# Kernel tuning notes

Hardware: AMD Instinct MI355X
Metric: run time of the kernel (lower is better)

The kernel has to match this reference:

```python
import jax, jax.numpy as jnp
import numpy as np


def setup_inputs() -> dict:
    key = jax.random.key(0)
    ks = jax.random.split(key, 8)
    B, QL, CL = 4, 128, 512
    XD, ED, D, YD = 64, 128, 128, 32
    sc = lambda fan_in: 1.0 / np.sqrt(fan_in)
    return {
        "q": jax.random.normal(ks[0], (B, QL, XD), jnp.float32),
        "f_embed": jax.random.normal(ks[1], (B, CL, ED), jnp.float32),
        "att_logits": jax.random.normal(ks[2], (B, QL, CL), jnp.float32),
        "W0": jax.random.normal(ks[3], (XD + ED, D), jnp.float32) * sc(XD + ED),
        "b0": jnp.zeros((D,), jnp.float32),
        "W1": jax.random.normal(ks[4], (D, D), jnp.float32) * sc(D),
        "b1": jnp.zeros((D,), jnp.float32),
        "Wo": jax.random.normal(ks[5], (D, YD), jnp.float32) * sc(D),
        "bo": jnp.zeros((YD,), jnp.float32),
    }


def reference(q, f_embed, att_logits, W0, b0, W1, b1, Wo, bo):
    # MultiInputDense on (qq, ff_embed): concat along last dim -> Dense(relu) x2 -> Dense(y_dim).
    # Split the first matmul so we never materialize the tiled concat:
    # concat([qq, ff]) @ W0 == qq @ W0[:xd] + ff @ W0[xd:]
    xd = q.shape[-1]
    q_part = jnp.einsum('bqx,xd->bqd', q, W0[:xd])          # [B, q_len, dim]
    f_part = jnp.einsum('bce,ed->bcd', f_embed, W0[xd:])    # [B, context_len, dim]
    h = jax.nn.relu(q_part[:, :, None, :] + f_part[:, None, :, :] + b0)  # [B,q,c,dim]
    h = jax.nn.relu(jnp.einsum('bqcd,de->bqce', h, W1) + b1)             # [B,q,c,dim]
    yy_hat = jnp.einsum('bqcd,dy->bqcy', h, Wo) + bo                     # [B,q,c,y_dim]
    att_map = jax.nn.softmax(att_logits, axis=-1)                        # [B,q,c]
    y_hat = jnp.einsum('bqc,bqcy->bqy', att_map, yy_hat)                 # [B,q,y_dim]
    return y_hat
```

## Files before the change

### kernel.cpp

```cpp
#include <hip/hip_runtime.h>

#define B_  4
#define QL  128
#define CL  512
#define XD  64
#define ED  128
#define DD  128
#define YD  32

typedef __attribute__((ext_vector_type(8))) _Float16 f16x8;
typedef __attribute__((ext_vector_type(4))) float f32x4;

__global__ void prep_kernel(const float* __restrict__ q,
                            const float* __restrict__ f,
                            const float* __restrict__ W0,
                            const float* __restrict__ b0,
                            const float* __restrict__ W1,
                            _Float16* __restrict__ fph,
                            _Float16* __restrict__ qph,
                            _Float16* __restrict__ w1f) {
  const int bid = blockIdx.x, tid = threadIdx.x;
  __shared__ float sbuf[256];
  if (bid < 1024) {
    const int sub = tid >> 7, d = tid & 127;
    const int row = bid * 2 + sub;
    sbuf[tid] = f[(size_t)row * ED + d];
    __syncthreads();
    float acc = 0.f;
    const float* w = W0 + XD * DD + d;
    const float* fr = sbuf + sub * 128;
    #pragma unroll 32
    for (int e = 0; e < ED; ++e) acc = fmaf(fr[e], w[e * DD], acc);
    fph[(size_t)row * DD + d] = (_Float16)acc;
  } else if (bid < 1280) {
    const int sub = tid >> 7, d = tid & 127;
    const int row = (bid - 1024) * 2 + sub;
    if (tid < 128) sbuf[tid] = q[((size_t)(bid - 1024) * 2 + (tid >> 6)) * XD + (tid & 63)];
    __syncthreads();
    float acc = b0[d];
    const float* w = W0 + d;
    const float* qr = sbuf + sub * 64;
    #pragma unroll 32
    for (int x = 0; x < XD; ++x) acc = fmaf(qr[x], w[x * DD], acc);
    qph[(size_t)row * DD + d] = (_Float16)acc;
  } else {
    #pragma unroll 8
    for (int i = 0; i < 64; ++i) {
      int idx = i * 256 + tid;
      int e = idx & 7;
      int lane = (idx >> 3) & 63;
      int jt = (idx >> 9) & 3;
      int kk = (idx >> 11) & 3;
      int wcol = (idx >> 13) & 1;
      int col = wcol * 64 + jt * 16 + (lane & 15);
      int k = kk * 32 + (lane >> 4) * 8 + e;
      w1f[idx] = (_Float16)W1[k * DD + col];
    }
  }
}

__launch_bounds__(256, 2)
__global__ void main_kernel(const float* __restrict__ logits,
                            const _Float16* __restrict__ fph,
                            const _Float16* __restrict__ qph,
                            const _Float16* __restrict__ w1f,
                            const float* __restrict__ b1,
                            const float* __restrict__ Wo,
                            const float* __restrict__ bo,
                            float* __restrict__ out) {
  __shared__ __align__(16) _Float16 h1[2][128 * 128];
  __shared__ float att[CL];
  __shared__ float g[4][DD];
  __shared__ float red[8];
  __shared__ float part[8][YD];

  const int tid = threadIdx.x;
  const int bid = blockIdx.x;
  const int wid = tid >> 6;
  const int ln  = tid & 63;
  const int b   = bid >> 7;
  const int wcol = wid & 1, wrow = wid >> 1;
  const int lhi = ln >> 4, llo = ln & 15;

  f16x8 wf[4][4];
  {
    const uint4* ws = (const uint4*)w1f;
    #pragma unroll
    for (int kk = 0; kk < 4; ++kk)
      #pragma unroll
      for (int jt = 0; jt < 4; ++jt) {
        uint4 v = ws[(((wcol * 4 + kk) * 4 + jt) << 6) + ln];
        wf[kk][jt] = *(const f16x8*)&v;
      }
  }
  uint4 qpv_u = ((const uint4*)(qph + (size_t)bid * DD))[tid & 15];
  const f16x8 qpv = *(const f16x8*)&qpv_u;

  ((float*)g)[tid] = 0.f;
  ((float*)g)[tid + 256] = 0.f;

  {
    const float* lg = logits + (size_t)bid * CL;
    float l0 = lg[tid], l1 = lg[tid + 256];
    float m = fmaxf(l0, l1);
    #pragma unroll
    for (int off = 1; off < 64; off <<= 1) m = fmaxf(m, __shfl_xor(m, off, 64));
    if (ln == 0) red[wid] = m;
    __syncthreads();
    m = fmaxf(fmaxf(red[0], red[1]), fmaxf(red[2], red[3]));
    float p0 = expf(l0 - m), p1 = expf(l1 - m);
    float s = p0 + p1;
    #pragma unroll
    for (int off = 1; off < 64; off <<= 1) s += __shfl_xor(s, off, 64);
    if (ln == 0) red[4 + wid] = s;
    __syncthreads();
    float inv = 1.f / (red[4] + red[5] + red[6] + red[7]);
    att[tid] = p0 * inv;
    att[tid + 256] = p1 * inv;
  }

  const int srow = tid >> 4;
  const int sg = tid & 15;
  const unsigned woff = (unsigned)(srow * 256 + ((sg * 16) ^ ((srow & 7) << 4)));

  uint4 sreg[8];
  auto stage_load = [&](int t) {
    const uint4* src = (const uint4*)(fph + ((size_t)b * CL + (size_t)t * 128) * DD);
    #pragma unroll
    for (int i = 0; i < 8; ++i) sreg[i] = src[i * 256 + tid];
  };
  auto stage_write = [&](int bufi) {
    char* base = (char*)&h1[bufi][0];
    const f16x8 zf = {};
    #pragma unroll
    for (int i = 0; i < 8; ++i) {
      f16x8 s = *(const f16x8*)&sreg[i] + qpv;
      s = __builtin_elementwise_max(s, zf);
      *(f16x8*)(base + i * 4096 + woff) = s;
    }
  };

  stage_load(0);
  stage_write(0);

  const int swz = (llo & 7) << 4;
  const int c0 = wrow * 64 + llo;
  const int j0 = wcol * 64 + llo;
  float b1v[4];
  #pragma unroll
  for (int jt = 0; jt < 4; ++jt) b1v[jt] = b1[j0 + jt * 16];
  float gp[4] = {0.f, 0.f, 0.f, 0.f};

  __syncthreads();

  for (int t = 0; t < 4; ++t) {
    if (t < 3) stage_load(t + 1);

    const char* hb = (const char*)&h1[t & 1][0];
    f32x4 acc[4][4];
    #pragma unroll
    for (int ct = 0; ct < 4; ++ct)
      #pragma unroll
      for (int jt = 0; jt < 4; ++jt) acc[ct][jt] = (f32x4){0.f, 0.f, 0.f, 0.f};

    #pragma unroll
    for (int kk = 0; kk < 4; ++kk) {
      const int kb = (kk * 64 + lhi * 16) ^ swz;
      f16x8 a[4];
      #pragma unroll
      for (int ct = 0; ct < 4; ++ct)
        a[ct] = *(const f16x8*)(hb + (c0 + ct * 16) * 256 + kb);
      #pragma unroll
      for (int ct = 0; ct < 4; ++ct)
        #pragma unroll
        for (int jt = 0; jt < 4; ++jt)
          acc[ct][jt] = __builtin_amdgcn_mfma_f32_16x16x32_f16(a[ct], wf[kk][jt], acc[ct][jt], 0, 0, 0);
    }

    const int cbase = t * 128 + wrow * 64 + lhi * 4;
    #pragma unroll
    for (int ct = 0; ct < 4; ++ct) {
      #pragma unroll
      for (int r = 0; r < 4; ++r) {
        float wv = att[cbase + ct * 16 + r];
        #pragma unroll
        for (int jt = 0; jt < 4; ++jt) {
          float h = fmaxf(acc[ct][jt][r] + b1v[jt], 0.f);
          gp[jt] = fmaf(wv, h, gp[jt]);
        }
      }
    }

    if (t < 3) stage_write((t + 1) & 1);
    __syncthreads();
  }

  #pragma unroll
  for (int jt = 0; jt < 4; ++jt) {
    gp[jt] += __shfl_xor(gp[jt], 16, 64);
    gp[jt] += __shfl_xor(gp[jt], 32, 64);
  }
  if (ln < 16) {
    #pragma unroll
    for (int jt = 0; jt < 4; ++jt) g[wid][j0 + jt * 16] = gp[jt];
  }
  __syncthreads();

  {
    int y = tid & 31, ch = tid >> 5;
    float a = 0.f;
    #pragma unroll
    for (int jj = 0; jj < 16; ++jj) {
      int j = ch * 16 + jj;
      float gj = g[0][j] + g[1][j] + g[2][j] + g[3][j];
      a = fmaf(gj, Wo[j * YD + y], a);
    }
    part[ch][y] = a;
  }
  __syncthreads();
  if (tid < YD) {
    float a = bo[tid];
    #pragma unroll
    for (int ch = 0; ch < 8; ++ch) a += part[ch][tid];
    out[(size_t)bid * YD + tid] = a;
  }
}

extern "C" void kernel_launch(void* const* d_in, const int* in_sizes, int n_in,
                              void* d_out, int out_size, void* d_ws, size_t ws_size,
                              hipStream_t stream) {
  const float* q  = (const float*)d_in[0];
  const float* f  = (const float*)d_in[1];
  const float* lg = (const float*)d_in[2];
  const float* W0 = (const float*)d_in[3];
  const float* b0 = (const float*)d_in[4];
  const float* W1 = (const float*)d_in[5];
  const float* b1 = (const float*)d_in[6];
  const float* Wo = (const float*)d_in[7];
  const float* bo = (const float*)d_in[8];
  float* out = (float*)d_out;

  _Float16* fph = (_Float16*)d_ws;
  _Float16* qph = fph + (size_t)B_ * CL * DD;
  _Float16* w1f = qph + (size_t)B_ * QL * DD;

  prep_kernel<<<1281, 256, 0, stream>>>(q, f, W0, b0, W1, fph, qph, w1f);
  main_kernel<<<B_ * QL, 256, 0, stream>>>(lg, fph, qph, w1f, b1, Wo, bo, out);
}
```

Measured before the change: 26.35 us.

## Load MFMA A-fragments directly from global and batch rows in prep kernel

The main kernel no longer stages the f-projection tile through double-buffered shared memory. Each lane now loads its A fragments straight from global (L2-resident) memory, applying the q bias and ReLU in registers. This removes the LDS writes and the per-tile barriers and frees 64KB of LDS for occupancy, at the cost of more global/L2 traffic per block. The prep kernel is restructured so each block computes 16 rows with register blocking, cutting the block count and redundant W0 reads. The attention weights are also read as vectors.

```diff
diff --git a/kernel.cpp b/kernel.cpp
--- a/kernel.cpp
+++ b/kernel.cpp
@@ -20,38 +20,65 @@
                             _Float16* __restrict__ qph,
                             _Float16* __restrict__ w1f) {
   const int bid = blockIdx.x, tid = threadIdx.x;
-  __shared__ float sbuf[256];
-  if (bid < 1024) {
-    const int sub = tid >> 7, d = tid & 127;
-    const int row = bid * 2 + sub;
-    sbuf[tid] = f[(size_t)row * ED + d];
-    __syncthreads();
-    float acc = 0.f;
+  __shared__ __align__(16) float fr[128][20];
+
+  if (bid < 128) {
+    const int r0 = bid * 16;
+    #pragma unroll
+    for (int i = 0; i < 8; ++i) {
+      int idx = i * 256 + tid;
+      fr[idx & 127][idx >> 7] = f[((size_t)r0 + (idx >> 7)) * ED + (idx & 127)];
+    }
+    __syncthreads();
+    const int d = tid & 127, half = tid >> 7;
+    float acc[8] = {};
     const float* w = W0 + XD * DD + d;
-    const float* fr = sbuf + sub * 128;
-    #pragma unroll 32
-    for (int e = 0; e < ED; ++e) acc = fmaf(fr[e], w[e * DD], acc);
-    fph[(size_t)row * DD + d] = (_Float16)acc;
-  } else if (bid < 1280) {
-    const int sub = tid >> 7, d = tid & 127;
-    const int row = (bid - 1024) * 2 + sub;
-    if (tid < 128) sbuf[tid] = q[((size_t)(bid - 1024) * 2 + (tid >> 6)) * XD + (tid & 63)];
-    __syncthreads();
-    float acc = b0[d];
+    for (int e = 0; e < ED; ++e) {
+      float wv = w[e * DD];
+      f32x4 f0 = *(const f32x4*)&fr[e][half * 8];
+      f32x4 f1 = *(const f32x4*)&fr[e][half * 8 + 4];
+      #pragma unroll
+      for (int j = 0; j < 4; ++j) {
+        acc[j]     = fmaf(f0[j], wv, acc[j]);
+        acc[j + 4] = fmaf(f1[j], wv, acc[j + 4]);
+      }
+    }
+    #pragma unroll
+    for (int j = 0; j < 8; ++j)
+      fph[((size_t)r0 + half * 8 + j) * DD + d] = (_Float16)acc[j];
+  } else if (bid < 160) {
+    const int r0 = (bid - 128) * 16;
+    #pragma unroll
+    for (int i = 0; i < 4; ++i) {
+      int idx = i * 256 + tid;
+      fr[idx & 63][idx >> 6] = q[((size_t)r0 + (idx >> 6)) * XD + (idx & 63)];
+    }
+    __syncthreads();
+    const int d = tid & 127, half = tid >> 7;
+    float acc[8];
+    float bv = b0[d];
+    #pragma unroll
+    for (int j = 0; j < 8; ++j) acc[j] = bv;
     const float* w = W0 + d;
-    const float* qr = sbuf + sub * 64;
-    #pragma unroll 32
-    for (int x = 0; x < XD; ++x) acc = fmaf(qr[x], w[x * DD], acc);
-    qph[(size_t)row * DD + d] = (_Float16)acc;
+    for (int e = 0; e < XD; ++e) {
+      float wv = w[e * DD];
+      f32x4 f0 = *(const f32x4*)&fr[e][half * 8];
+      f32x4 f1 = *(const f32x4*)&fr[e][half * 8 + 4];
+      #pragma unroll
+      for (int j = 0; j < 4; ++j) {
+        acc[j]     = fmaf(f0[j], wv, acc[j]);
+        acc[j + 4] = fmaf(f1[j], wv, acc[j + 4]);
+      }
+    }
+    #pragma unroll
+    for (int j = 0; j < 8; ++j)
+      qph[((size_t)r0 + half * 8 + j) * DD + d] = (_Float16)acc[j];
   } else {
     #pragma unroll 8
     for (int i = 0; i < 64; ++i) {
       int idx = i * 256 + tid;
-      int e = idx & 7;
-      int lane = (idx >> 3) & 63;
-      int jt = (idx >> 9) & 3;
-      int kk = (idx >> 11) & 3;
-      int wcol = (idx >> 13) & 1;
+      int e = idx & 7, lane = (idx >> 3) & 63, jt = (idx >> 9) & 3;
+      int kk = (idx >> 11) & 3, wcol = (idx >> 13) & 1;
       int col = wcol * 64 + jt * 16 + (lane & 15);
       int k = kk * 32 + (lane >> 4) * 8 + e;
       w1f[idx] = (_Float16)W1[k * DD + col];
@@ -68,7 +95,6 @@
                             const float* __restrict__ Wo,
                             const float* __restrict__ bo,
                             float* __restrict__ out) {
-  __shared__ __align__(16) _Float16 h1[2][128 * 128];
   __shared__ float att[CL];
   __shared__ float g[4][DD];
   __shared__ float red[8];
@@ -93,8 +119,17 @@
         wf[kk][jt] = *(const f16x8*)&v;
       }
   }
-  uint4 qpv_u = ((const uint4*)(qph + (size_t)bid * DD))[tid & 15];
-  const f16x8 qpv = *(const f16x8*)&qpv_u;
+  f16x8 qpv[4];
+  {
+    const uint4* qs = (const uint4*)(qph + (size_t)bid * DD);
+    #pragma unroll
+    for (int kk = 0; kk < 4; ++kk) {
+      uint4 v = qs[kk * 2 + (lhi >> 1) * 0 + 0];
+      (void)v;
+      uint4 u = qs[(kk * 32 + lhi * 8) >> 3];
+      qpv[kk] = *(const f16x8*)&u;
+    }
+  }
 
   ((float*)g)[tid] = 0.f;
   ((float*)g)[tid + 256] = 0.f;
@@ -118,58 +153,35 @@
     att[tid] = p0 * inv;
     att[tid + 256] = p1 * inv;
   }
-
-  const int srow = tid >> 4;
-  const int sg = tid & 15;
-  const unsigned woff = (unsigned)(srow * 256 + ((sg * 16) ^ ((srow & 7) << 4)));
-
-  uint4 sreg[8];
-  auto stage_load = [&](int t) {
-    const uint4* src = (const uint4*)(fph + ((size_t)b * CL + (size_t)t * 128) * DD);
-    #pragma unroll
-    for (int i = 0; i < 8; ++i) sreg[i] = src[i * 256 + tid];
-  };
-  auto stage_write = [&](int bufi) {
-    char* base = (char*)&h1[bufi][0];
-    const f16x8 zf = {};
-    #pragma unroll
-    for (int i = 0; i < 8; ++i) {
-      f16x8 s = *(const f16x8*)&sreg[i] + qpv;
-      s = __builtin_elementwise_max(s, zf);
-      *(f16x8*)(base + i * 4096 + woff) = s;
-    }
-  };
-
-  stage_load(0);
-  stage_write(0);
-
-  const int swz = (llo & 7) << 4;
-  const int c0 = wrow * 64 + llo;
+  __syncthreads();
+
   const int j0 = wcol * 64 + llo;
   float b1v[4];
   #pragma unroll
   for (int jt = 0; jt < 4; ++jt) b1v[jt] = b1[j0 + jt * 16];
   float gp[4] = {0.f, 0.f, 0.f, 0.f};
 
-  __syncthreads();
-
+  const _Float16* abase = fph + ((size_t)b * CL) * DD + ((size_t)(wrow * 64 + llo)) * DD + lhi * 8;
+  const f16x8 zf = {};
+
+  #pragma unroll
   for (int t = 0; t < 4; ++t) {
-    if (t < 3) stage_load(t + 1);
-
-    const char* hb = (const char*)&h1[t & 1][0];
     f32x4 acc[4][4];
     #pragma unroll
     for (int ct = 0; ct < 4; ++ct)
       #pragma unroll
       for (int jt = 0; jt < 4; ++jt) acc[ct][jt] = (f32x4){0.f, 0.f, 0.f, 0.f};
 
+    const _Float16* at = abase + (size_t)t * 128 * DD;
     #pragma unroll
     for (int kk = 0; kk < 4; ++kk) {
-      const int kb = (kk * 64 + lhi * 16) ^ swz;
       f16x8 a[4];
       #pragma unroll
-      for (int ct = 0; ct < 4; ++ct)
-        a[ct] = *(const f16x8*)(hb + (c0 + ct * 16) * 256 + kb);
+      for (int ct = 0; ct < 4; ++ct) {
+        uint4 v = *(const uint4*)(at + (size_t)ct * 16 * DD + kk * 32);
+        f16x8 x = *(const f16x8*)&v + qpv[kk];
+        a[ct] = __builtin_elementwise_max(x, zf);
+      }
       #pragma unroll
       for (int ct = 0; ct < 4; ++ct)
         #pragma unroll
@@ -180,19 +192,16 @@
     const int cbase = t * 128 + wrow * 64 + lhi * 4;
     #pragma unroll
     for (int ct = 0; ct < 4; ++ct) {
+      f32x4 a4 = *(const f32x4*)&att[cbase + ct * 16];
       #pragma unroll
       for (int r = 0; r < 4; ++r) {
-        float wv = att[cbase + ct * 16 + r];
         #pragma unroll
         for (int jt = 0; jt < 4; ++jt) {
           float h = fmaxf(acc[ct][jt][r] + b1v[jt], 0.f);
-          gp[jt] = fmaf(wv, h, gp[jt]);
+          gp[jt] = fmaf(a4[r], h, gp[jt]);
         }
       }
     }
-
-    if (t < 3) stage_write((t + 1) & 1);
-    __syncthreads();
   }
 
   #pragma unroll
@@ -244,6 +253,6 @@
   _Float16* qph = fph + (size_t)B_ * CL * DD;
   _Float16* w1f = qph + (size_t)B_ * QL * DD;
 
-  prep_kernel<<<1281, 256, 0, stream>>>(q, f, W0, b0, W1, fph, qph, w1f);
+  prep_kernel<<<161, 256, 0, stream>>>(q, f, W0, b0, W1, fph, qph, w1f);
   main_kernel<<<B_ * QL, 256, 0, stream>>>(lg, fph, qph, w1f, b1, Wo, bo, out);
 }
```

Result: slower. 29.96 us (+13.7%).
